# Kernel tuning notes

Hardware: AMD Instinct MI355X
Metric: run time of the kernel (lower is better)

## Reference

```python
import jax, jax.numpy as jnp
import numpy as np

DIM = 1024
NE = 4            # num_experts
MLP = 4           # mlp_ratio
H = 16            # num_heads
HD = DIM // H     # head dim
EXP = 3 * DIM + MLP * DIM   # expand output dim (7*dim)
CIN = DIM + MLP * DIM       # contract input dim (5*dim)


def layer_norm(x, g, b, eps=1e-5):
    m = jnp.mean(x, axis=-1, keepdims=True)
    v = jnp.var(x, axis=-1, keepdims=True)
    return (x - m) * jax.lax.rsqrt(v + eps) * g + b


def setup_inputs() -> dict:
    key = jax.random.key(0)
    ks = jax.random.split(key, 8)
    B, N = 8, 1024
    x = jax.random.normal(ks[0], (B, N, DIM), jnp.float32)
    expert_mask = jax.random.randint(ks[1], (B, N), 0, NE, jnp.int32)
    router_probs = jax.random.uniform(ks[2], (B, N, NE), jnp.float32)
    expand_weight = jax.random.normal(ks[3], (EXP, DIM), jnp.float32) * 0.02
    mlp_bias = jnp.zeros((MLP * DIM,), jnp.float32)
    contract_weight = jax.random.normal(ks[4], (2 * DIM, CIN), jnp.float32) * 0.02
    contract_bias = jnp.zeros((2 * DIM,), jnp.float32)
    norm1_g = jnp.ones((DIM,), jnp.float32)
    norm1_b = jnp.zeros((DIM,), jnp.float32)
    norm2_g = jnp.ones((DIM,), jnp.float32)
    norm2_b = jnp.zeros((DIM,), jnp.float32)
    alpha = jnp.zeros((1,), jnp.float32)
    return dict(x=x, expert_mask=expert_mask, router_probs=router_probs,
                expand_weight=expand_weight, mlp_bias=mlp_bias,
                contract_weight=contract_weight, contract_bias=contract_bias,
                norm1_g=norm1_g, norm1_b=norm1_b, norm2_g=norm2_g, norm2_b=norm2_b,
                alpha=alpha)


def reference(x, expert_mask, router_probs, expand_weight, mlp_bias,
              contract_weight, contract_bias, norm1_g, norm1_b,
              norm2_g, norm2_b, alpha):
    B, N, _ = x.shape
    shift = (NE - 1 - expert_mask).astype(jnp.int32)          # [B,N]
    # nested (matryoshka) active dims per token
    d_in = DIM // jnp.left_shift(1, shift)                    # expand: active input dims
    d_out = (2 * DIM) // jnp.left_shift(1, shift)             # contract: active output dims

    # nested_linear_expand: zero inactive input features, then full GEMM
    in_mask = (jnp.arange(DIM) < d_in[..., None]).astype(x.dtype)
    xn = layer_norm(x, norm1_g, norm1_b) * in_mask
    y = jnp.einsum('bnd,od->bno', xn, expand_weight)          # [B,N,7*dim]

    qkv = y[..., :3 * DIM]
    mlp_hidden = y[..., 3 * DIM:] + mlp_bias

    q = qkv[..., :DIM]
    k = layer_norm(qkv[..., DIM:2 * DIM], norm2_g, norm2_b)
    v = layer_norm(qkv[..., 2 * DIM:], norm2_g, norm2_b)

    qh = q.reshape(B, N, H, HD)
    kh = k.reshape(B, N, H, HD)
    vh = v.reshape(B, N, H, HD)
    scale = HD ** -0.5
    attn = jax.nn.softmax(jnp.einsum('bqhd,bkhd->bhqk', qh, kh) * scale, axis=-1)
    attn_out = jnp.einsum('bhqk,bkhd->bqhd', attn, vh).reshape(B, N, DIM)

    h = jnp.concatenate([attn_out, jax.nn.gelu(mlp_hidden, approximate=False)], axis=-1)
    # nested_linear_contract: full GEMM, zero inactive output features
    z = jnp.einsum('bnc,oc->bno', h, contract_weight) + contract_bias  # [B,N,2*dim]
    z = z * (jnp.arange(2 * DIM) < d_out[..., None]).astype(z.dtype)

    attn_o = z[..., :DIM] + x
    mlp_o = z[..., DIM:]
    expert_probs = jnp.take_along_axis(router_probs, expert_mask[..., None].astype(jnp.int32), axis=-1)  # [B,N,1]
    out = attn_o + (alpha * expert_probs + 1.0) * mlp_o
    return (out, expert_mask, router_probs)
```

## Files before the change

kernel.cpp:

```cpp
#include <hip/hip_runtime.h>
#include <hip/hip_bf16.h>
#include <math.h>

typedef __bf16 bf16_t;
typedef __attribute__((ext_vector_type(8))) __bf16 bf16x8;
typedef __attribute__((ext_vector_type(4))) __bf16 bf16x4;
typedef __attribute__((ext_vector_type(4))) float f32x4;
typedef __attribute__((ext_vector_type(4))) unsigned u32x4;

typedef __attribute__((address_space(1))) unsigned as1u;
typedef __attribute__((address_space(3))) unsigned as3u;

#define MAXT1 68
#define MAXJ2 2112

__device__ __forceinline__ void async_copy16(bf16_t* lds, const bf16_t* g) {
  __builtin_amdgcn_global_load_lds((as1u*)g, (as3u*)lds, 16, 0, 0);
}

__device__ __forceinline__ float gelu_exact(float t) {
  return 0.5f * t * (1.0f + erff(t * 0.70710678118654752f));
}

__device__ __forceinline__ unsigned pack_bf16(float a, float b) {
  unsigned short ha = __builtin_bit_cast(unsigned short, (bf16_t)a);
  unsigned short hb = __builtin_bit_cast(unsigned short, (bf16_t)b);
  return (unsigned)ha | ((unsigned)hb << 16);
}

__global__ __launch_bounds__(256)
void cast_kernel(const float* __restrict__ w, bf16_t* __restrict__ o, int n) {
  int i = (blockIdx.x * 256 + threadIdx.x) * 4;
  if (i < n) {
    float4 v = *(const float4*)(w + i);
    bf16x4 t;
    t[0] = (bf16_t)v.x; t[1] = (bf16_t)v.y; t[2] = (bf16_t)v.z; t[3] = (bf16_t)v.w;
    *(bf16x4*)(o + i) = t;
  }
}

__global__ __launch_bounds__(1024)
void sort_kernel(const int* __restrict__ em, int* __restrict__ perm,
                 int* __restrict__ t1, int* __restrict__ j2) {
  __shared__ int cnt[4], cur[4], tb[5], jb[5];
  const int tid = threadIdx.x;
  const int wave = tid >> 6, lane = tid & 63;
  if (tid < 4) cnt[tid] = 0;
  __syncthreads();
  for (int c = wave; c < 128; c += 16) {
    int e = em[c * 64 + lane];
    unsigned long long m0 = __ballot(e == 0), m1 = __ballot(e == 1);
    unsigned long long m2 = __ballot(e == 2), m3 = __ballot(e == 3);
    if (lane == 0) {
      atomicAdd(&cnt[0], (int)__popcll(m0)); atomicAdd(&cnt[1], (int)__popcll(m1));
      atomicAdd(&cnt[2], (int)__popcll(m2)); atomicAdd(&cnt[3], (int)__popcll(m3));
    }
  }
  __syncthreads();
  if (tid == 0) {
    cur[0] = 0; cur[1] = cnt[0]; cur[2] = cnt[0] + cnt[1]; cur[3] = cnt[0] + cnt[1] + cnt[2];
    tb[0] = 0; jb[0] = 0;
    for (int i = 0; i < 4; ++i) {
      int e = 3 - i;
      tb[i + 1] = tb[i] + ((cnt[e] + 127) >> 7);
    }
    for (int e = 0; e < 4; ++e) {
      int nt = (cnt[e] + 127) >> 7;
      jb[e + 1] = jb[e] + nt * (4 << e);
    }
  }
  __syncthreads();
  for (int c = wave; c < 128; c += 16) {
    int i = c * 64 + lane;
    int e = em[i];
    unsigned long long m0 = __ballot(e == 0), m1 = __ballot(e == 1);
    unsigned long long m2 = __ballot(e == 2), m3 = __ballot(e == 3);
    unsigned long long me = e == 0 ? m0 : e == 1 ? m1 : e == 2 ? m2 : m3;
    int bl = 0;
    if (lane < 4) {
      unsigned long long ml = lane == 0 ? m0 : lane == 1 ? m1 : lane == 2 ? m2 : m3;
      bl = atomicAdd(&cur[lane], (int)__popcll(ml));
    }
    int base = __shfl(bl, e);
    unsigned long long lt = (1ull << lane) - 1ull;
    perm[base + (int)__popcll(me & lt)] = i;
  }
  int offp[5];
  offp[0] = 0;
  #pragma unroll
  for (int e = 0; e < 4; ++e) offp[e + 1] = offp[e] + cnt[e];
  for (int t = tid; t < MAXT1; t += 1024) {
    int e = -1, loc = 0;
    #pragma unroll
    for (int i = 0; i < 4; ++i) if (t >= tb[i] && t < tb[i + 1]) { e = 3 - i; loc = t - tb[i]; }
    if (e >= 0) {
      t1[t * 3] = e; t1[t * 3 + 1] = offp[e] + loc * 128;
      t1[t * 3 + 2] = min(128, cnt[e] - loc * 128);
    } else t1[t * 3] = -1;
  }
  for (int j = tid; j < MAXJ2; j += 1024) {
    int e = -1, loc = 0;
    #pragma unroll
    for (int q = 0; q < 4; ++q) if (j >= jb[q] && j < jb[q + 1]) { e = q; loc = j - jb[q]; }
    if (e >= 0) {
      int t = loc >> (2 + e), b = loc & ((4 << e) - 1);
      j2[j * 4] = e; j2[j * 4 + 1] = offp[e] + t * 128;
      j2[j * 4 + 2] = min(128, cnt[e] - t * 128); j2[j * 4 + 3] = b;
    } else j2[j * 4] = -1;
  }
}

__global__ __launch_bounds__(256)
void ln1_kernel(const float* __restrict__ x, const float* __restrict__ gam,
                const float* __restrict__ bet, const int* __restrict__ em,
                bf16_t* __restrict__ xn) {
  const int row = blockIdx.x, tid = threadIdx.x;
  const float4 v = ((const float4*)(x + (size_t)row * 1024))[tid];
  float s = v.x + v.y + v.z + v.w;
  float sq = v.x * v.x + v.y * v.y + v.z * v.z + v.w * v.w;
  #pragma unroll
  for (int off = 1; off < 64; off <<= 1) { s += __shfl_xor(s, off); sq += __shfl_xor(sq, off); }
  __shared__ float red[8];
  const int wave = tid >> 6, lane = tid & 63;
  if (lane == 0) { red[wave] = s; red[4 + wave] = sq; }
  __syncthreads();
  s = red[0] + red[1] + red[2] + red[3];
  sq = red[4] + red[5] + red[6] + red[7];
  const float mean = s * (1.0f / 1024.0f);
  const float var = sq * (1.0f / 1024.0f) - mean * mean;
  const float rstd = rsqrtf(var + 1e-5f);
  const int din = 1024 >> (3 - em[row]);
  const float4 gv = ((const float4*)gam)[tid];
  const float4 bv = ((const float4*)bet)[tid];
  const int c0 = tid * 4;
  float vf[4] = {v.x, v.y, v.z, v.w};
  float gf[4] = {gv.x, gv.y, gv.z, gv.w};
  float bvf[4] = {bv.x, bv.y, bv.z, bv.w};
  bf16x4 o;
  #pragma unroll
  for (int i = 0; i < 4; ++i) {
    float t = (vf[i] - mean) * rstd * gf[i] + bvf[i];
    o[i] = (c0 + i < din) ? (bf16_t)t : (bf16_t)0.0f;
  }
  *(bf16x4*)(xn + (size_t)row * 1024 + c0) = o;
}

__global__ __launch_bounds__(256)
void ln2_kernel(bf16_t* __restrict__ kv, const float* __restrict__ gam,
                const float* __restrict__ bet) {
  const int row = blockIdx.x, tid = threadIdx.x;
  bf16_t* base = kv + (size_t)row * 2048;
  bf16x4 kk = *(const bf16x4*)(base + tid * 4);
  bf16x4 vv = *(const bf16x4*)(base + 1024 + tid * 4);
  float kf[4], vf[4];
  float ks = 0, ksq = 0, vs = 0, vsq = 0;
  #pragma unroll
  for (int i = 0; i < 4; ++i) {
    kf[i] = (float)kk[i]; ks += kf[i]; ksq += kf[i] * kf[i];
    vf[i] = (float)vv[i]; vs += vf[i]; vsq += vf[i] * vf[i];
  }
  #pragma unroll
  for (int off = 1; off < 64; off <<= 1) {
    ks += __shfl_xor(ks, off); ksq += __shfl_xor(ksq, off);
    vs += __shfl_xor(vs, off); vsq += __shfl_xor(vsq, off);
  }
  __shared__ float red[16];
  const int wave = tid >> 6, lane = tid & 63;
  if (lane == 0) { red[wave] = ks; red[4 + wave] = ksq; red[8 + wave] = vs; red[12 + wave] = vsq; }
  __syncthreads();
  ks = red[0] + red[1] + red[2] + red[3];
  ksq = red[4] + red[5] + red[6] + red[7];
  vs = red[8] + red[9] + red[10] + red[11];
  vsq = red[12] + red[13] + red[14] + red[15];
  const float mk = ks * (1.f / 1024.f), mv = vs * (1.f / 1024.f);
  const float rk = rsqrtf(ksq * (1.f / 1024.f) - mk * mk + 1e-5f);
  const float rv = rsqrtf(vsq * (1.f / 1024.f) - mv * mv + 1e-5f);
  const float4 gv = ((const float4*)gam)[tid];
  const float4 bv = ((const float4*)bet)[tid];
  float gf[4] = {gv.x, gv.y, gv.z, gv.w}, bvf[4] = {bv.x, bv.y, bv.z, bv.w};
  bf16x4 ko, vo;
  #pragma unroll
  for (int i = 0; i < 4; ++i) {
    ko[i] = (bf16_t)((kf[i] - mk) * rk * gf[i] + bvf[i]);
    vo[i] = (bf16_t)((vf[i] - mv) * rv * gf[i] + bvf[i]);
  }
  *(bf16x4*)(base + tid * 4) = ko;
  *(bf16x4*)(base + 1024 + tid * 4) = vo;
}

__global__ __launch_bounds__(256)
void vt_kernel(const bf16_t* __restrict__ kv, bf16_t* __restrict__ vT) {
  __shared__ bf16_t t[64][80];
  const int tt = blockIdx.x, head = blockIdx.y;
  const int tid = threadIdx.x;
  const int r8 = tid >> 3, c8 = tid & 7;
  #pragma unroll
  for (int i = 0; i < 2; ++i) {
    const int tok = i * 32 + r8;
    bf16x8 v = *(const bf16x8*)(kv + (size_t)(tt * 64 + tok) * 2048 + 1024 + head * 64 + c8 * 8);
    #pragma unroll
    for (int j = 0; j < 8; ++j) t[c8 * 8 + j][tok] = v[j];
  }
  __syncthreads();
  const int bb = tt >> 4;
  const int tloc = (tt & 15) * 64;
  #pragma unroll
  for (int i = 0; i < 2; ++i) {
    const int d = i * 32 + r8;
    bf16x8 v = *(const bf16x8*)(&t[d][c8 * 8]);
    *(bf16x8*)(vT + (size_t)((bb * 16 + head) * 64 + d) * 1024 + tloc + c8 * 8) = v;
  }
}

template<int EPI>
__global__ __launch_bounds__(256)
void gemm_bt(const bf16_t* __restrict__ A, const bf16_t* __restrict__ W,
             const int* __restrict__ perm, const int* __restrict__ desc,
             const float* __restrict__ bias,
             bf16_t* __restrict__ hb, bf16_t* __restrict__ kvb,
             bf16_t* __restrict__ z) {
  constexpr int K = (EPI == 0) ? 1024 : 5120;
  constexpr int BN = (EPI == 0) ? 128 : 64;
  constexpr int NI = BN / 32;
  constexpr int WC = BN / 2;
  const int* d = desc + ((EPI == 0) ? blockIdx.y * 3 : blockIdx.x * 4);
  const int e = d[0];
  if (e < 0) return;
  const int nval = d[2];
  const int bn = (EPI == 0) ? blockIdx.x : d[3];
  const int nkt = (EPI == 0) ? (2 << e) : 80;

  __shared__ bf16_t SMEM[17408];
  __shared__ int prow[128];
  bf16_t* As = SMEM;
  bf16_t* Bs = SMEM + 8192;

  const int tid = threadIdx.x;
  if (tid < 128) prow[tid] = perm[d[1] + min(tid, nval - 1)];
  const int wave = tid >> 6, lane = tid & 63;
  const int l15 = lane & 15, l4 = lane >> 4;
  const int wm = wave >> 1, wn = wave & 1;

  f32x4 acc[4][NI] = {};

  const int rbase = tid >> 3;
  const int ss = (tid & 7) ^ (rbase & 7);
  __syncthreads();
  const bf16_t* Ag[4];
  #pragma unroll
  for (int i = 0; i < 4; ++i) Ag[i] = A + (size_t)prow[i * 32 + rbase] * K + ss * 8;
  const bf16_t* Wg = W + (size_t)(bn * BN + rbase) * K + ss * 8;

  for (int kt = 0; kt < nkt; ++kt) {
    #pragma unroll
    for (int i = 0; i < 4; ++i)
      async_copy16(As + (i * 256 + wave * 64) * 8, Ag[i] + kt * 64);
    #pragma unroll
    for (int i = 0; i < NI; ++i)
      async_copy16(Bs + (i * 256 + wave * 64) * 8, Wg + (size_t)(i * 32) * K + kt * 64);
    __syncthreads();
    #pragma unroll
    for (int ks = 0; ks < 2; ++ks) {
      bf16x8 a[4], b[NI];
      #pragma unroll
      for (int mi = 0; mi < 4; ++mi) {
        const int r = wm * 64 + mi * 16 + l15;
        const int slot = (ks * 4 + l4) ^ (r & 7);
        a[mi] = *(const bf16x8*)(As + r * 64 + slot * 8);
      }
      #pragma unroll
      for (int ni = 0; ni < NI; ++ni) {
        const int r = wn * WC + ni * 16 + l15;
        const int slot = (ks * 4 + l4) ^ (r & 7);
        b[ni] = *(const bf16x8*)(Bs + r * 64 + slot * 8);
      }
      #pragma unroll
      for (int mi = 0; mi < 4; ++mi)
        #pragma unroll
        for (int ni = 0; ni < NI; ++ni)
          acc[mi][ni] = __builtin_amdgcn_mfma_f32_16x16x32_bf16(a[mi], b[ni], acc[mi][ni], 0, 0, 0);
    }
    __syncthreads();
  }

  #pragma unroll
  for (int mi = 0; mi < 4; ++mi) {
    #pragma unroll
    for (int ni = 0; ni < NI; ++ni) {
      const int colf = wn * WC + ni * 16 + l15;
      #pragma unroll
      for (int r = 0; r < 4; ++r) {
        const int row = wm * 64 + mi * 16 + l4 * 4 + r;
        const float c = acc[mi][ni][r];
        bf16_t v;
        if (EPI == 0) {
          const int gc = bn * 128 + colf;
          v = (gc >= 3072) ? (bf16_t)gelu_exact(c + bias[gc - 3072]) : (bf16_t)c;
        } else {
          v = (bf16_t)(c + bias[bn * 64 + colf]);
        }
        SMEM[row * 136 + colf] = v;
      }
    }
  }
  __syncthreads();
  if (EPI == 0) {
    const int col0 = (tid & 15) * 8;
    const int gc0 = bn * 128 + col0;
    #pragma unroll
    for (int i = 0; i < 8; ++i) {
      const int row = (tid >> 4) * 8 + i;
      if (row < nval) {
        const size_t token = (size_t)prow[row];
        bf16x8 v = *(const bf16x8*)(SMEM + row * 136 + col0);
        if (gc0 < 1024)      *(bf16x8*)(hb + token * 5120 + gc0) = v;
        else if (gc0 < 3072) *(bf16x8*)(kvb + token * 2048 + (gc0 - 1024)) = v;
        else                 *(bf16x8*)(hb + token * 5120 + 1024 + (gc0 - 3072)) = v;
      }
    }
  } else {
    const int col0 = (tid & 7) * 8;
    const int gc0 = bn * 64 + col0;
    #pragma unroll
    for (int i = 0; i < 4; ++i) {
      const int row = (tid >> 3) * 4 + i;
      if (row < nval) {
        const size_t token = (size_t)prow[row];
        bf16x8 v = *(const bf16x8*)(SMEM + row * 136 + col0);
        *(bf16x8*)(z + token * 2048 + gc0) = v;
      }
    }
  }
}

__global__ __launch_bounds__(256)
void attn_kernel(const bf16_t* __restrict__ kv, const bf16_t* __restrict__ vT,
                 bf16_t* __restrict__ hb) {
  __shared__ bf16_t Kl[64 * 64];
  __shared__ bf16_t Vl[64 * 64];
  const int tid = threadIdx.x;
  const int wave = tid >> 6, lane = tid & 63;
  const int l15 = lane & 15, l4 = lane >> 4;
  const int qt = blockIdx.x, bh = blockIdx.y;
  const int bb = bh >> 4;
  const int tok0 = bb << 10;
  const int d0 = (bh & 15) << 6;

  const int qrow = tok0 + qt * 64 + wave * 16 + l15;
  const bf16x8 bq0 = *(const bf16x8*)(hb + (size_t)qrow * 5120 + d0 + l4 * 8);
  const bf16x8 bq1 = *(const bf16x8*)(hb + (size_t)qrow * 5120 + d0 + 32 + l4 * 8);

  f32x4 o[4] = {};
  float mrun = -1e30f, lrun = 0.f;

  const int krb = tid >> 3;
  const int kss = (tid & 7) ^ (krb & 7);
  const int idx0 = ((2 * (l4 & 1) + 0) * 16 + l15) * 4;
  const int idx1 = ((2 * (l4 & 1) + 1) * 16 + l15) * 4;
  const bool hi = (l4 >> 1) != 0;

  for (int kt = 0; kt < 16; ++kt) {
    const int krow0 = tok0 + kt * 64;
    #pragma unroll
    for (int i = 0; i < 2; ++i) {
      async_copy16(Kl + (i * 256 + wave * 64) * 8,
                   kv + (size_t)(krow0 + i * 32 + krb) * 2048 + d0 + kss * 8);
      async_copy16(Vl + (i * 256 + wave * 64) * 8,
                   vT + (size_t)(bh * 64 + i * 32 + krb) * 1024 + kt * 64 + kss * 8);
    }
    __syncthreads();

    f32x4 s[4] = {};
    #pragma unroll
    for (int ks = 0; ks < 2; ++ks) {
      const bf16x8 bq = ks ? bq1 : bq0;
      #pragma unroll
      for (int kc = 0; kc < 4; ++kc) {
        const int r = kc * 16 + l15;
        const int slot = (ks * 4 + l4) ^ (r & 7);
        bf16x8 ak = *(const bf16x8*)(Kl + r * 64 + slot * 8);
        s[kc] = __builtin_amdgcn_mfma_f32_16x16x32_bf16(ak, bq, s[kc], 0, 0, 0);
      }
    }

    float mx = s[0][0];
    #pragma unroll
    for (int kc = 0; kc < 4; ++kc)
      #pragma unroll
      for (int r = 0; r < 4; ++r) mx = fmaxf(mx, s[kc][r]);
    mx = fmaxf(mx, __shfl_xor(mx, 16));
    mx = fmaxf(mx, __shfl_xor(mx, 32));
    mx *= 0.125f;
    const float mnew = fmaxf(mrun, mx);
    const float corr = __expf(mrun - mnew);
    float ps = 0.f;
    #pragma unroll
    for (int kc = 0; kc < 4; ++kc)
      #pragma unroll
      for (int r = 0; r < 4; ++r) {
        const float p = __expf(s[kc][r] * 0.125f - mnew);
        s[kc][r] = p;
        ps += p;
      }
    ps += __shfl_xor(ps, 16);
    ps += __shfl_xor(ps, 32);
    lrun = lrun * corr + ps;
    mrun = mnew;

    unsigned pd[4][2], bp[4][2][2];
    #pragma unroll
    for (int kc = 0; kc < 4; ++kc) {
      pd[kc][0] = pack_bf16(s[kc][0], s[kc][1]);
      pd[kc][1] = pack_bf16(s[kc][2], s[kc][3]);
    }
    #pragma unroll
    for (int kc = 0; kc < 4; ++kc)
      #pragma unroll
      for (int rp = 0; rp < 2; ++rp) {
        bp[kc][rp][0] = (unsigned)__builtin_amdgcn_ds_bpermute(idx0, (int)pd[kc][rp]);
        bp[kc][rp][1] = (unsigned)__builtin_amdgcn_ds_bpermute(idx1, (int)pd[kc][rp]);
      }
    u32x4 w0, w1;
    w0[0] = hi ? bp[1][0][0] : bp[0][0][0];
    w0[1] = hi ? bp[1][1][0] : bp[0][1][0];
    w0[2] = hi ? bp[1][0][1] : bp[0][0][1];
    w0[3] = hi ? bp[1][1][1] : bp[0][1][1];
    w1[0] = hi ? bp[3][0][0] : bp[2][0][0];
    w1[1] = hi ? bp[3][1][0] : bp[2][1][0];
    w1[2] = hi ? bp[3][0][1] : bp[2][0][1];
    w1[3] = hi ? bp[3][1][1] : bp[2][1][1];
    const bf16x8 pa0 = __builtin_bit_cast(bf16x8, w0);
    const bf16x8 pa1 = __builtin_bit_cast(bf16x8, w1);

    float cq[4];
    #pragma unroll
    for (int r = 0; r < 4; ++r) cq[r] = __shfl(corr, l4 * 4 + r);
    #pragma unroll
    for (int dn = 0; dn < 4; ++dn)
      #pragma unroll
      for (int r = 0; r < 4; ++r) o[dn][r] *= cq[r];

    #pragma unroll
    for (int dn = 0; dn < 4; ++dn) {
      const int r = dn * 16 + l15;
      bf16x8 bv0 = *(const bf16x8*)(Vl + r * 64 + ((l4 ^ (r & 7)) * 8));
      bf16x8 bv1 = *(const bf16x8*)(Vl + r * 64 + (((4 + l4) ^ (r & 7)) * 8));
      o[dn] = __builtin_amdgcn_mfma_f32_16x16x32_bf16(pa0, bv0, o[dn], 0, 0, 0);
      o[dn] = __builtin_amdgcn_mfma_f32_16x16x32_bf16(pa1, bv1, o[dn], 0, 0, 0);
    }
    __syncthreads();
  }

  const float il = 1.0f / lrun;
  float linv[4];
  #pragma unroll
  for (int r = 0; r < 4; ++r) linv[r] = __shfl(il, l4 * 4 + r);
  #pragma unroll
  for (int r = 0; r < 4; ++r) {
    const int gq = tok0 + qt * 64 + wave * 16 + l4 * 4 + r;
    #pragma unroll
    for (int dn = 0; dn < 4; ++dn)
      hb[(size_t)gq * 5120 + d0 + dn * 16 + l15] = (bf16_t)(o[dn][r] * linv[r]);
  }
}

__global__ __launch_bounds__(256)
void final_kernel(const bf16_t* __restrict__ z, const float* __restrict__ x,
                  const int* __restrict__ em, const float* __restrict__ rp,
                  const float* __restrict__ alpha, float* __restrict__ out) {
  const int row = blockIdx.x, tid = threadIdx.x;
  const int e = em[row];
  const int dout = 2048 >> (3 - e);
  const float f = alpha[0] * rp[row * 4 + e] + 1.0f;
  const bf16x4 z0 = ((const bf16x4*)(z + (size_t)row * 2048))[tid];
  const bf16x4 z1 = ((const bf16x4*)(z + (size_t)row * 2048 + 1024))[tid];
  const float4 xv = ((const float4*)(x + (size_t)row * 1024))[tid];
  const int c = tid * 4;
  float4 o;
  o.x = ((c + 0) < dout ? (float)z0[0] : 0.f) + xv.x + f * ((1024 + c + 0) < dout ? (float)z1[0] : 0.f);
  o.y = ((c + 1) < dout ? (float)z0[1] : 0.f) + xv.y + f * ((1024 + c + 1) < dout ? (float)z1[1] : 0.f);
  o.z = ((c + 2) < dout ? (float)z0[2] : 0.f) + xv.z + f * ((1024 + c + 2) < dout ? (float)z1[2] : 0.f);
  o.w = ((c + 3) < dout ? (float)z0[3] : 0.f) + xv.w + f * ((1024 + c + 3) < dout ? (float)z1[3] : 0.f);
  ((float4*)(out + (size_t)row * 1024))[tid] = o;
  float* out_em = out + 8388608;
  float* out_rp = out_em + 8192;
  if (tid == 0) out_em[row] = (float)e;
  if (tid < 4) out_rp[row * 4 + tid] = rp[row * 4 + tid];
}

extern "C" void kernel_launch(void* const* d_in, const int* in_sizes, int n_in,
                              void* d_out, int out_size, void* d_ws, size_t ws_size,
                              hipStream_t stream) {
  const float* x = (const float*)d_in[0];
  const int* em = (const int*)d_in[1];
  const float* rp = (const float*)d_in[2];
  const float* w_exp = (const float*)d_in[3];
  const float* mlp_bias = (const float*)d_in[4];
  const float* w_con = (const float*)d_in[5];
  const float* c_bias = (const float*)d_in[6];
  const float* n1g = (const float*)d_in[7];
  const float* n1b = (const float*)d_in[8];
  const float* n2g = (const float*)d_in[9];
  const float* n2b = (const float*)d_in[10];
  const float* alpha = (const float*)d_in[11];

  char* ws = (char*)d_ws;
  bf16_t* Wexp = (bf16_t*)ws;
  bf16_t* xn   = (bf16_t*)(ws + 14680064);
  bf16_t* vT   = (bf16_t*)(ws + 14680064);
  int*    perm = (int*)(ws + 31457280);
  int*    t1d  = (int*)(ws + 31457280 + 32768);
  int*    j2d  = (int*)(ws + 31457280 + 34816);
  bf16_t* kvb  = (bf16_t*)(ws + 48234496);
  bf16_t* z    = (bf16_t*)(ws + 48234496);
  bf16_t* Wcon = (bf16_t*)(ws + 81788928);
  bf16_t* hb   = (bf16_t*)(ws + 102760448);

  sort_kernel<<<1, 1024, 0, stream>>>(em, perm, t1d, j2d);
  cast_kernel<<<7168, 256, 0, stream>>>(w_exp, Wexp, 7340032);
  cast_kernel<<<10240, 256, 0, stream>>>(w_con, Wcon, 10485760);
  ln1_kernel<<<8192, 256, 0, stream>>>(x, n1g, n1b, em, xn);
  gemm_bt<0><<<dim3(56, MAXT1), 256, 0, stream>>>(xn, Wexp, perm, t1d, mlp_bias,
                                                  hb, kvb, nullptr);
  ln2_kernel<<<8192, 256, 0, stream>>>(kvb, n2g, n2b);
  vt_kernel<<<dim3(128, 16), 256, 0, stream>>>(kvb, vT);
  attn_kernel<<<dim3(16, 128), 256, 0, stream>>>(kvb, vT, hb);
  gemm_bt<1><<<MAXJ2, 256, 0, stream>>>(hb, Wcon, perm, j2d, c_bias,
                                        nullptr, nullptr, z);
  final_kernel<<<8192, 256, 0, stream>>>(z, x, em, rp, alpha, (float*)d_out);
}
```

Baseline: 439.4 us.

## Double-buffer GEMM LDS tiles, reorder contract blocks by expert, prioritize attention MFMAs

The GEMM kernel now keeps two LDS stages: the next k-tile is loaded asynchronously while the current one is computed, leaving one barrier per iteration instead of a load-then-wait pattern. The contract-GEMM block descriptors are now ordered starting from the largest expert, so the heaviest blocks launch first and tail imbalance shrinks. The attention kernel raises wave priority (s_setprio) around its MFMA sections. The cost is that the GEMM uses twice the LDS per block, which may reduce how many blocks fit on each CU.

Result: no change. 439.3 us (-0.0%).

```diff
diff --git a/kernel.cpp b/kernel.cpp
--- a/kernel.cpp
+++ b/kernel.cpp
@@ -62,11 +62,9 @@
     tb[0] = 0; jb[0] = 0;
     for (int i = 0; i < 4; ++i) {
       int e = 3 - i;
-      tb[i + 1] = tb[i] + ((cnt[e] + 127) >> 7);
-    }
-    for (int e = 0; e < 4; ++e) {
       int nt = (cnt[e] + 127) >> 7;
-      jb[e + 1] = jb[e] + nt * (4 << e);
+      tb[i + 1] = tb[i] + nt;
+      jb[i + 1] = jb[i] + nt * (4 << e);
     }
   }
   __syncthreads();
@@ -101,7 +99,7 @@
   for (int j = tid; j < MAXJ2; j += 1024) {
     int e = -1, loc = 0;
     #pragma unroll
-    for (int q = 0; q < 4; ++q) if (j >= jb[q] && j < jb[q + 1]) { e = q; loc = j - jb[q]; }
+    for (int i = 0; i < 4; ++i) if (j >= jb[i] && j < jb[i + 1]) { e = 3 - i; loc = j - jb[i]; }
     if (e >= 0) {
       int t = loc >> (2 + e), b = loc & ((4 << e) - 1);
       j2[j * 4] = e; j2[j * 4 + 1] = offp[e] + t * 128;
@@ -212,6 +210,17 @@
   }
 }
 
+#define STAGE(BUF, KT) do { \
+    bf16_t* As_ = SMEM + (BUF) * BUFE; \
+    bf16_t* Bs_ = As_ + 8192; \
+    _Pragma("unroll") \
+    for (int i_ = 0; i_ < 4; ++i_) \
+      async_copy16(As_ + (i_ * 256 + wave * 64) * 8, Ag[i_] + (KT) * 64); \
+    _Pragma("unroll") \
+    for (int i_ = 0; i_ < NI; ++i_) \
+      async_copy16(Bs_ + (i_ * 256 + wave * 64) * 8, Wg + (size_t)(i_ * 32) * K + (size_t)(KT) * 64); \
+  } while (0)
+
 template<int EPI>
 __global__ __launch_bounds__(256)
 void gemm_bt(const bf16_t* __restrict__ A, const bf16_t* __restrict__ W,
@@ -223,6 +232,7 @@
   constexpr int BN = (EPI == 0) ? 128 : 64;
   constexpr int NI = BN / 32;
   constexpr int WC = BN / 2;
+  constexpr int BUFE = 8192 + BN * 64;
   const int* d = desc + ((EPI == 0) ? blockIdx.y * 3 : blockIdx.x * 4);
   const int e = d[0];
   if (e < 0) return;
@@ -230,11 +240,8 @@
   const int bn = (EPI == 0) ? blockIdx.x : d[3];
   const int nkt = (EPI == 0) ? (2 << e) : 80;
 
-  __shared__ bf16_t SMEM[17408];
+  __shared__ bf16_t SMEM[2 * BUFE];
   __shared__ int prow[128];
-  bf16_t* As = SMEM;
-  bf16_t* Bs = SMEM + 8192;
-
   const int tid = threadIdx.x;
   if (tid < 128) prow[tid] = perm[d[1] + min(tid, nval - 1)];
   const int wave = tid >> 6, lane = tid & 63;
@@ -251,14 +258,13 @@
   for (int i = 0; i < 4; ++i) Ag[i] = A + (size_t)prow[i * 32 + rbase] * K + ss * 8;
   const bf16_t* Wg = W + (size_t)(bn * BN + rbase) * K + ss * 8;
 
+  STAGE(0, 0);
+  __syncthreads();
+
   for (int kt = 0; kt < nkt; ++kt) {
-    #pragma unroll
-    for (int i = 0; i < 4; ++i)
-      async_copy16(As + (i * 256 + wave * 64) * 8, Ag[i] + kt * 64);
-    #pragma unroll
-    for (int i = 0; i < NI; ++i)
-      async_copy16(Bs + (i * 256 + wave * 64) * 8, Wg + (size_t)(i * 32) * K + kt * 64);
-    __syncthreads();
+    if (kt + 1 < nkt) STAGE((kt + 1) & 1, kt + 1);
+    const bf16_t* Asr = SMEM + (kt & 1) * BUFE;
+    const bf16_t* Bsr = Asr + 8192;
     #pragma unroll
     for (int ks = 0; ks < 2; ++ks) {
       bf16x8 a[4], b[NI];
@@ -266,13 +272,13 @@
       for (int mi = 0; mi < 4; ++mi) {
         const int r = wm * 64 + mi * 16 + l15;
         const int slot = (ks * 4 + l4) ^ (r & 7);
-        a[mi] = *(const bf16x8*)(As + r * 64 + slot * 8);
+        a[mi] = *(const bf16x8*)(Asr + r * 64 + slot * 8);
       }
       #pragma unroll
       for (int ni = 0; ni < NI; ++ni) {
         const int r = wn * WC + ni * 16 + l15;
         const int slot = (ks * 4 + l4) ^ (r & 7);
-        b[ni] = *(const bf16x8*)(Bs + r * 64 + slot * 8);
+        b[ni] = *(const bf16x8*)(Bsr + r * 64 + slot * 8);
       }
       #pragma unroll
       for (int mi = 0; mi < 4; ++mi)
@@ -371,6 +377,7 @@
     __syncthreads();
 
     f32x4 s[4] = {};
+    __builtin_amdgcn_s_setprio(1);
     #pragma unroll
     for (int ks = 0; ks < 2; ++ks) {
       const bf16x8 bq = ks ? bq1 : bq0;
@@ -382,6 +389,7 @@
         s[kc] = __builtin_amdgcn_mfma_f32_16x16x32_bf16(ak, bq, s[kc], 0, 0, 0);
       }
     }
+    __builtin_amdgcn_s_setprio(0);
 
     float mx = s[0][0];
     #pragma unroll
@@ -440,6 +448,7 @@
       #pragma unroll
       for (int r = 0; r < 4; ++r) o[dn][r] *= cq[r];
 
+    __builtin_amdgcn_s_setprio(1);
     #pragma unroll
     for (int dn = 0; dn < 4; ++dn) {
       const int r = dn * 16 + l15;
@@ -448,6 +457,7 @@
       o[dn] = __builtin_amdgcn_mfma_f32_16x16x32_bf16(pa0, bv0, o[dn], 0, 0, 0);
       o[dn] = __builtin_amdgcn_mfma_f32_16x16x32_bf16(pa1, bv1, o[dn], 0, 0, 0);
     }
+    __builtin_amdgcn_s_setprio(0);
     __syncthreads();
   }
 
```
